# Kernel optimization log

Hardware: AMD Instinct MI355X
Metric: run time of the kernel (lower is better)

The kernel has to match this reference:

```python
import jax, jax.numpy as jnp
import numpy as np

def setup_inputs() -> dict:
    key = jax.random.key(0)
    x = jax.random.normal(key, (2, 16, 2048, 64), dtype=jnp.float32)
    return {"x": x}

def reference(x):
    # Unnormalized attention: scores = q k^T (no softmax, no scaling), out = scores v,
    # with q = k = v = x. Faithful to the two torch.einsum calls.
    scores = jnp.einsum('bhid,bhjd->bhij', x, x)   # [B,H,T,T]
    out = jnp.einsum('bhij,bhjd->bhid', scores, x)  # [B,H,T,D]
    return out
```

## Files before the change

kernel.cpp:

```cpp
#include <hip/hip_runtime.h>


#define TDIM 2048
#define DDIM 64
#define NHEADS 32
#define NCH 16

typedef float f4 __attribute__((ext_vector_type(4)));
typedef float f32x4 __attribute__((ext_vector_type(4)));
typedef short bf16x8 __attribute__((ext_vector_type(8)));
typedef short s4 __attribute__((ext_vector_type(4)));

__device__ __forceinline__ void async_copy16(const void* g, void* l) {
    __builtin_amdgcn_global_load_lds(
        (const __attribute__((address_space(1))) void*)g,
        (__attribute__((address_space(3))) void*)l, 16, 0, 0);
}

__device__ __forceinline__ short f2bf(float f) {
    unsigned u = __builtin_bit_cast(unsigned, f);
    unsigned r = (u + 0x7fffu + ((u >> 16) & 1u)) >> 16;
    return (short)r;
}
__device__ __forceinline__ float bf2f(short s) {
    return __builtin_bit_cast(float, ((unsigned)(unsigned short)s) << 16);
}

__device__ __forceinline__ const bf16x8* fragp(const short* base, int row,
                                               int rowlen, int kelem) {
    const char* p = (const char*)(base + row * rowlen);
    return (const bf16x8*)(p + ((kelem * 2) ^ ((row & 7) << 4)));
}

__global__ __launch_bounds__(512) void k1_gram(const float* __restrict__ x,
                                               short* __restrict__ part,
                                               short* __restrict__ xbf) {
    __shared__ __align__(16) short XT[64 * 128];

    const int b    = blockIdx.x;
    const int tid  = threadIdx.x;
    const int lane = tid & 63;
    const int w    = tid >> 6;
    const int head = b >> 4, ch = b & 15;

    const float* xh = x + ((size_t)head * TDIM + ch * 128) * DDIM;

    const int rg = tid >> 4;
    const int cg = tid & 15;
    const int r0 = rg * 4, c4 = cg * 4;

    f4 v[4];
#pragma unroll
    for (int k = 0; k < 4; ++k)
        v[k] = *reinterpret_cast<const f4*>(xh + (size_t)(r0 + k) * DDIM + c4);

    short pk[4][4];
#pragma unroll
    for (int k = 0; k < 4; ++k)
#pragma unroll
        for (int j = 0; j < 4; ++j) pk[k][j] = f2bf(v[k][j]);

#pragma unroll
    for (int j = 0; j < 4; ++j) {
        const int c = c4 + j;
        s4 t4;
#pragma unroll
        for (int k = 0; k < 4; ++k) t4[k] = pk[k][j];
        *(s4*)((char*)XT + c * 256 + ((2 * r0) ^ ((c & 7) << 4))) = t4;
    }

    {
        char* img = (char*)xbf + (size_t)head * 262144;
#pragma unroll
        for (int k = 0; k < 4; ++k) {
            const int R = ch * 128 + r0 + k;
            s4 t4;
#pragma unroll
            for (int j = 0; j < 4; ++j) t4[j] = pk[k][j];
            *(s4*)(img + (size_t)R * 128 + ((2 * c4) ^ ((R & 7) << 4))) = t4;
        }
    }
    __syncthreads();

    const int li = lane & 15, g = lane >> 4;
    const int i_tile = w >> 1, j0 = (w & 1) * 2;

    f32x4 acc[2];
#pragma unroll
    for (int d = 0; d < 2; ++d) acc[d] = (f32x4){0.f, 0.f, 0.f, 0.f};

#pragma unroll
    for (int k0 = 0; k0 < 128; k0 += 32) {
        bf16x8 af, bv[2];
        af = *fragp(XT, i_tile * 16 + li, 128, k0 + 8 * g);
        bv[0] = *fragp(XT, (j0 + 0) * 16 + li, 128, k0 + 8 * g);
        bv[1] = *fragp(XT, (j0 + 1) * 16 + li, 128, k0 + 8 * g);
#pragma unroll
        for (int d = 0; d < 2; ++d)
            acc[d] = __builtin_amdgcn_mfma_f32_16x16x32_bf16(
                af, bv[d], acc[d], 0, 0, 0);
    }

    short* pp = part + (size_t)b * 4096;
#pragma unroll
    for (int d = 0; d < 2; ++d) {
        s4 o;
#pragma unroll
        for (int q = 0; q < 4; ++q) o[q] = f2bf(acc[d][q]);
        *(s4*)(pp + (((w * 2 + d) * 64 + lane) << 2)) = o;
    }
}

__global__ __launch_bounds__(256) void k2a_reduce(const short* __restrict__ part,
                                                  short* __restrict__ gbf) {
    const int b    = blockIdx.x;
    const int tid  = threadIdx.x;
    const int head = b >> 2, quarter = b & 3;

    const int f = quarter * 256 + tid;
    const short* ph = part + (size_t)head * NCH * 4096 + (f << 2);

    float s[4] = {0.f, 0.f, 0.f, 0.f};
#pragma unroll
    for (int c = 0; c < NCH; ++c) {
        const s4 v = *reinterpret_cast<const s4*>(ph + (size_t)c * 4096);
#pragma unroll
        for (int q = 0; q < 4; ++q) s[q] += bf2f(v[q]);
    }

    const int lane = f & 63, wd = f >> 6;
    const int w = wd >> 1, d = wd & 1;
    const int g = lane >> 4, li = lane & 15;
    const int i_tile = w >> 1, j_tile = (w & 1) * 2 + d;
    const int j = j_tile * 16 + li;
    char* gb = (char*)gbf + (size_t)head * 8192;
#pragma unroll
    for (int q = 0; q < 4; ++q) {
        const int i = i_tile * 16 + g * 4 + q;
        *(short*)(gb + i * 128 + ((2 * j) ^ ((i & 7) << 4))) = f2bf(s[q]);
    }
}

__global__ __launch_bounds__(256) void k2b_xg(float* __restrict__ out,
                                              const short* __restrict__ xbf,
                                              const short* __restrict__ gbf) {
    __shared__ __align__(16) short Xb[4096];
    __shared__ __align__(16) short Gb[4096];

    const int b    = blockIdx.x;
    const int tid  = threadIdx.x;
    const int lane = tid & 63;
    const int w    = tid >> 6;
    const int head = b >> 5, ch = b & 31;

    {
        const short* gx = xbf + (size_t)head * 131072 + ch * 4096 +
                          w * 1024 + lane * 8;
        const short* gg = gbf + (size_t)head * 4096 + w * 1024 + lane * 8;
#pragma unroll
        for (int it = 0; it < 2; ++it) {
            async_copy16(gx + it * 512, Xb + w * 1024 + it * 512);
            async_copy16(gg + it * 512, Gb + w * 1024 + it * 512);
        }
    }
    __syncthreads();

    const int li = lane & 15, g = lane >> 4;

    f32x4 acc[4];
#pragma unroll
    for (int d = 0; d < 4; ++d) acc[d] = (f32x4){0.f, 0.f, 0.f, 0.f};

#pragma unroll
    for (int k0 = 0; k0 < 64; k0 += 32) {
        bf16x8 af, bv[4];
        af = *fragp(Xb, w * 16 + li, 64, k0 + 8 * g);
#pragma unroll
        for (int d = 0; d < 4; ++d)
            bv[d] = *fragp(Gb, d * 16 + li, 64, k0 + 8 * g);
#pragma unroll
        for (int d = 0; d < 4; ++d)
            acc[d] = __builtin_amdgcn_mfma_f32_16x16x32_bf16(
                af, bv[d], acc[d], 0, 0, 0);
    }

    float* oh = out + ((size_t)head * TDIM + ch * 64) * DDIM;
#pragma unroll
    for (int d = 0; d < 4; ++d)
#pragma unroll
        for (int q = 0; q < 4; ++q)
            oh[(w * 16 + g * 4 + q) * 64 + d * 16 + li] = acc[d][q];
}

extern "C" void kernel_launch(void* const* d_in, const int* in_sizes, int n_in,
                              void* d_out, int out_size, void* d_ws, size_t ws_size,
                              hipStream_t stream) {
    const float* x = (const float*)d_in[0];
    float* out  = (float*)d_out;
    short* part = (short*)d_ws;
    short* gbf  = part + (size_t)512 * 4096;
    short* xbf  = gbf + (size_t)NHEADS * 4096;

    k1_gram<<<NHEADS * NCH, 512, 0, stream>>>(x, part, xbf);
    k2a_reduce<<<128, 256, 0, stream>>>(part, gbf);
    k2b_xg<<<NHEADS * 32, 256, 0, stream>>>(out, xbf, gbf);
}
```

Baseline: 22.63 us.

## Drop bf16 X staging buffer; convert fp32 X directly in second-stage kernel

```diff
diff --git a/kernel.cpp b/kernel.cpp
--- a/kernel.cpp
+++ b/kernel.cpp
@@ -33,8 +33,7 @@
 }
 
 __global__ __launch_bounds__(512) void k1_gram(const float* __restrict__ x,
-                                               short* __restrict__ part,
-                                               short* __restrict__ xbf) {
+                                               short* __restrict__ part) {
     __shared__ __align__(16) short XT[64 * 128];
 
     const int b    = blockIdx.x;
@@ -54,31 +53,13 @@
     for (int k = 0; k < 4; ++k)
         v[k] = *reinterpret_cast<const f4*>(xh + (size_t)(r0 + k) * DDIM + c4);
 
-    short pk[4][4];
-#pragma unroll
-    for (int k = 0; k < 4; ++k)
-#pragma unroll
-        for (int j = 0; j < 4; ++j) pk[k][j] = f2bf(v[k][j]);
-
 #pragma unroll
     for (int j = 0; j < 4; ++j) {
-        const int c = c4 + j;
         s4 t4;
 #pragma unroll
-        for (int k = 0; k < 4; ++k) t4[k] = pk[k][j];
+        for (int k = 0; k < 4; ++k) t4[k] = f2bf(v[k][j]);
+        const int c = c4 + j;
         *(s4*)((char*)XT + c * 256 + ((2 * r0) ^ ((c & 7) << 4))) = t4;
-    }
-
-    {
-        char* img = (char*)xbf + (size_t)head * 262144;
-#pragma unroll
-        for (int k = 0; k < 4; ++k) {
-            const int R = ch * 128 + r0 + k;
-            s4 t4;
-#pragma unroll
-            for (int j = 0; j < 4; ++j) t4[j] = pk[k][j];
-            *(s4*)(img + (size_t)R * 128 + ((2 * c4) ^ ((R & 7) << 4))) = t4;
-        }
     }
     __syncthreads();
 
@@ -141,27 +122,34 @@
     }
 }
 
-__global__ __launch_bounds__(256) void k2b_xg(float* __restrict__ out,
-                                              const short* __restrict__ xbf,
+__global__ __launch_bounds__(512) void k2b_xg(const float* __restrict__ x,
+                                              float* __restrict__ out,
                                               const short* __restrict__ gbf) {
-    __shared__ __align__(16) short Xb[4096];
+    __shared__ __align__(16) short Xb[8192];
     __shared__ __align__(16) short Gb[4096];
 
     const int b    = blockIdx.x;
     const int tid  = threadIdx.x;
     const int lane = tid & 63;
     const int w    = tid >> 6;
-    const int head = b >> 5, ch = b & 31;
+    const int head = b >> 4, ch = b & 15;
 
     {
-        const short* gx = xbf + (size_t)head * 131072 + ch * 4096 +
-                          w * 1024 + lane * 8;
-        const short* gg = gbf + (size_t)head * 4096 + w * 1024 + lane * 8;
+        const short* gg = gbf + (size_t)head * 4096 + w * 512 + lane * 8;
+        async_copy16(gg, Gb + w * 512);
+    }
+
+    const float* xh = x + ((size_t)head * TDIM + ch * 128) * DDIM;
 #pragma unroll
-        for (int it = 0; it < 2; ++it) {
-            async_copy16(gx + it * 512, Xb + w * 1024 + it * 512);
-            async_copy16(gg + it * 512, Gb + w * 1024 + it * 512);
-        }
+    for (int e = 0; e < 4; ++e) {
+        const int i4 = e * 512 + tid;
+        const int r  = i4 >> 4;
+        const int c4 = (i4 & 15) << 2;
+        const f4 v = *reinterpret_cast<const f4*>(xh + (size_t)i4 * 4);
+        s4 pk;
+        pk[0] = f2bf(v[0]); pk[1] = f2bf(v[1]);
+        pk[2] = f2bf(v[2]); pk[3] = f2bf(v[3]);
+        *(s4*)((char*)Xb + r * 128 + ((2 * c4) ^ ((r & 7) << 4))) = pk;
     }
     __syncthreads();
 
@@ -184,7 +172,7 @@
                 af, bv[d], acc[d], 0, 0, 0);
     }
 
-    float* oh = out + ((size_t)head * TDIM + ch * 64) * DDIM;
+    float* oh = out + ((size_t)head * TDIM + ch * 128) * DDIM;
 #pragma unroll
     for (int d = 0; d < 4; ++d)
 #pragma unroll
@@ -199,9 +187,8 @@
     float* out  = (float*)d_out;
     short* part = (short*)d_ws;
     short* gbf  = part + (size_t)512 * 4096;
-    short* xbf  = gbf + (size_t)NHEADS * 4096;
 
-    k1_gram<<<NHEADS * NCH, 512, 0, stream>>>(x, part, xbf);
+    k1_gram<<<NHEADS * NCH, 512, 0, stream>>>(x, part);
     k2a_reduce<<<128, 256, 0, stream>>>(part, gbf);
-    k2b_xg<<<NHEADS * 32, 256, 0, stream>>>(out, xbf, gbf);
+    k2b_xg<<<512, 512, 0, stream>>>(x, out, gbf);
 }
```

New measurement: 18.85 us. 16.7% less time.
